# Kernel tuning notes

Hardware: AMD Instinct MI355X
Metric: run time of the kernel (lower is better)

Reference implementation:

```python
import math
import jax, jax.numpy as jnp
import numpy as np

B, S, D, H, DK = 2, 2048, 1024, 16, 64
NUM_BUCKETS, MAX_DISTANCE = 32, 128


def _relative_position_bucket(rel_pos):
    # bidirectional=True (encoder): is_decoder=False
    nb = NUM_BUCKETS // 2
    rel_buckets = (rel_pos > 0).astype(jnp.int32) * nb
    rp = jnp.abs(rel_pos)
    max_exact = nb // 2
    is_small = rp < max_exact
    rp_large = max_exact + (
        jnp.log(rp.astype(jnp.float32) / max_exact)
        / math.log(MAX_DISTANCE / max_exact)
        * (nb - max_exact)
    ).astype(jnp.int32)
    rp_large = jnp.minimum(rp_large, nb - 1)
    return rel_buckets + jnp.where(is_small, rp, rp_large)


def compute_bias(rel_bias, q_len, k_len):
    ctx = jnp.arange(q_len, dtype=jnp.int32)[:, None]
    mem = jnp.arange(k_len, dtype=jnp.int32)[None, :]
    buckets = _relative_position_bucket(mem - ctx)          # [q,k]
    vals = rel_bias[buckets]                                 # [q,k,H]
    return jnp.transpose(vals, (2, 0, 1))[None]              # [1,H,q,k]


def setup_inputs() -> dict:
    key = jax.random.key(0)
    ks = jax.random.split(key, 6)
    scale = 0.02
    return {
        "hidden_states": jax.random.normal(ks[0], (B, S, D), jnp.float32),
        "Wq": jax.random.normal(ks[1], (D, H * DK), jnp.float32) * scale,
        "Wk": jax.random.normal(ks[2], (D, H * DK), jnp.float32) * scale,
        "Wv": jax.random.normal(ks[3], (D, H * DK), jnp.float32) * scale,
        "Wo": jax.random.normal(ks[4], (H * DK, D), jnp.float32) * scale,
        "rel_bias": jax.random.normal(ks[5], (NUM_BUCKETS, H), jnp.float32) * scale,
    }


def reference(hidden_states, Wq, Wk, Wv, Wo, rel_bias):
    b, s, _ = hidden_states.shape

    def shape(x):  # [b,s,H*DK] -> [b,H,s,DK]
        return x.reshape(b, s, H, DK).transpose(0, 2, 1, 3)

    q = shape(hidden_states @ Wq)
    k = shape(hidden_states @ Wk)
    v = shape(hidden_states @ Wv)

    # T5: no 1/sqrt(d_k) scaling
    scores = jnp.einsum("bhqd,bhkd->bhqk", q, k)
    position_bias = compute_bias(rel_bias, s, s)             # [1,H,s,s]
    scores = scores + position_bias
    attn = jax.nn.softmax(scores.astype(jnp.float32), axis=-1).astype(scores.dtype)
    out = jnp.einsum("bhqk,bhkd->bhqd", attn, v)
    out = out.transpose(0, 2, 1, 3).reshape(b, s, H * DK)
    return out @ Wo
```

## Files before the change

kernel.cpp:

```cpp
#include <hip/hip_runtime.h>

#define HH 16
#define DKK 64
#define SS 2048
#define BB 2
#define DD 1024

typedef __attribute__((ext_vector_type(4))) float f32x4;
typedef __attribute__((ext_vector_type(8))) short bf16x8;
typedef __attribute__((ext_vector_type(4))) short s16x4;
typedef __attribute__((ext_vector_type(2))) int i32x2;

#define WAITCNT_VM0 0xF70

__device__ __forceinline__ short bf16b(float f) {
    union { float f; unsigned u; } x; x.f = f;
    unsigned r = (x.u + 0x7fffu + ((x.u >> 16) & 1u)) >> 16;
    return (short)r;
}

__device__ __forceinline__ unsigned f2u(float f) {
    union { float f; unsigned u; } x; x.f = f;
    return x.u;
}

__device__ __forceinline__ f32x4 mfma16(bf16x8 a, bf16x8 b, f32x4 c) {
    return __builtin_amdgcn_mfma_f32_16x16x32_bf16(a, b, c, 0, 0, 0);
}

__device__ __forceinline__ void lds16(const short* g, short* l) {
    __builtin_amdgcn_global_load_lds(
        (const __attribute__((address_space(1))) void*)g,
        (__attribute__((address_space(3))) void*)l, 16, 0, 0);
}

__global__ __launch_bounds__(256) void prep(
    const float* __restrict__ hs,
    const float* __restrict__ W0, const float* __restrict__ W1,
    const float* __restrict__ W2, const float* __restrict__ W3,
    const float* __restrict__ rb,
    short* __restrict__ hsb,
    short* __restrict__ T0, short* __restrict__ T1,
    short* __restrict__ T2, short* __restrict__ T3,
    float* __restrict__ tab) {
    __shared__ short tile[32][33];
    int blk = blockIdx.x, tid = threadIdx.x;
    if (blk < 4096) {
        int i = (blk * 256 + tid) * 4;
        f32x4 v = *(const f32x4*)(hs + i);
        s16x4 o;
        o.x = bf16b(v.x); o.y = bf16b(v.y); o.z = bf16b(v.z); o.w = bf16b(v.w);
        *(s16x4*)(hsb + i) = o;
    } else if (blk < 8192) {
        int t = blk - 4096;
        int z = t >> 10, r = t & 1023;
        int bx = r & 31, by = r >> 5;
        const float* W; short* T;
        switch (z) {
            case 0: W = W0; T = T0; break;
            case 1: W = W1; T = T1; break;
            case 2: W = W2; T = T2; break;
            default: W = W3; T = T3; break;
        }
        int n0 = bx * 32, k0 = by * 32;
        int tx = tid & 31, ty = (tid >> 5) * 4;
#pragma unroll
        for (int i = 0; i < 4; i++)
            tile[ty + i][tx] = bf16b(W[(k0 + ty + i) * DD + n0 + tx]);
        __syncthreads();
#pragma unroll
        for (int i = 0; i < 4; i++)
            T[(n0 + ty + i) * DD + k0 + tx] = tile[tx][ty + i];
    } else {
        int idx = (blk - 8192) * 256 + tid;
        if (idx < HH * 4095) {
            int h = idx / 4095, d = idx % 4095;
            int rel = d - 2047;
            int bucket = (rel > 0) ? 16 : 0;
            unsigned rr = (rel < 0) ? (unsigned)(-rel) : (unsigned)rel;
            int add;
            if (rr < 8) add = (int)rr;
            else {
                int e = 31 - __clz(rr);
                unsigned long long r2 = (unsigned long long)rr * (unsigned long long)rr;
                int f = 2 * e + ((r2 >= (2ull << (2 * e))) ? 1 : 0);
                add = 8 + (f - 6);
                if (add > 15) add = 15;
            }
            bucket += add;
            tab[h * 4095 + d] = rb[bucket * HH + h] * 1.44269504f;
        }
    }
}

__global__ __launch_bounds__(256) void gemm_qkv(
    const short* __restrict__ A, const short* __restrict__ Wt,
    short* __restrict__ Cq, short* __restrict__ Ck, short* __restrict__ Cvt) {
    const int K = 1024;
    __shared__ short As[128 * 32];
    __shared__ short Bs[128 * 32];
    int tid = threadIdx.x;
    int wave = tid >> 6, lane = tid & 63;
    int quad = lane >> 4, l16 = lane & 15;
    int m0 = blockIdx.y * 128, n0 = blockIdx.x * 128;

    int wm = (wave & 1) * 64, wn = (wave >> 1) * 64;
    int r0 = tid >> 2, c0 = (tid & 3) * 8;

    f32x4 acc[4][4];
#pragma unroll
    for (int i = 0; i < 4; i++)
#pragma unroll
        for (int j = 0; j < 4; j++) acc[i][j] = (f32x4){0.f, 0.f, 0.f, 0.f};

    for (int k0 = 0; k0 < K; k0 += 32) {
        __syncthreads();
        lds16(A + (size_t)(m0 + r0) * K + k0 + c0, As + wave * 512);
        lds16(A + (size_t)(m0 + 64 + r0) * K + k0 + c0, As + 2048 + wave * 512);
        lds16(Wt + (size_t)(n0 + r0) * K + k0 + c0, Bs + wave * 512);
        lds16(Wt + (size_t)(n0 + 64 + r0) * K + k0 + c0, Bs + 2048 + wave * 512);
        __syncthreads();
        bf16x8 af[4], bfr[4];
#pragma unroll
        for (int t = 0; t < 4; t++) {
            af[t] = *(const bf16x8*)(As + (wm + t * 16 + l16) * 32 + quad * 8);
            bfr[t] = *(const bf16x8*)(Bs + (wn + t * 16 + l16) * 32 + quad * 8);
        }
#pragma unroll
        for (int mt = 0; mt < 4; mt++)
#pragma unroll
            for (int nt = 0; nt < 4; nt++)
                acc[mt][nt] = mfma16(af[mt], bfr[nt], acc[mt][nt]);
    }

#pragma unroll
    for (int mt = 0; mt < 4; mt++) {
#pragma unroll
        for (int nt = 0; nt < 4; nt++) {
#pragma unroll
            for (int r = 0; r < 4; r++) {
                int gm = m0 + wm + mt * 16 + quad * 4 + r;
                int gn = n0 + wn + nt * 16 + l16;
                int b = gm >> 11, s = gm & 2047;
                int which = gn >> 10;
                int h = (gn >> 6) & 15, dk = gn & 63;
                short bv = bf16b(acc[mt][nt][r]);
                if (which == 0)
                    Cq[(((size_t)(b * HH + h)) * SS + s) * DKK + dk] = bv;
                else if (which == 1)
                    Ck[(((size_t)(b * HH + h)) * SS + s) * DKK + dk] = bv;
                else
                    Cvt[(((size_t)(b * HH + h)) * DKK + dk) * SS + s] = bv;
            }
        }
    }
}

__global__ __launch_bounds__(256) void gemm_out(
    const short* __restrict__ A, const short* __restrict__ Wt,
    float* __restrict__ Cout) {
    const int K = 1024, N = 1024;
    __shared__ short As[64 * 32];
    __shared__ short Bs[128 * 32];
    int tid = threadIdx.x;
    int wave = tid >> 6, lane = tid & 63;
    int quad = lane >> 4, l16 = lane & 15;
    int m0 = blockIdx.y * 64, n0 = blockIdx.x * 128;

    int wm = (wave & 1) * 32, wn = (wave >> 1) * 64;
    int r0 = tid >> 2, c0 = (tid & 3) * 8;

    f32x4 acc[2][4];
#pragma unroll
    for (int i = 0; i < 2; i++)
#pragma unroll
        for (int j = 0; j < 4; j++) acc[i][j] = (f32x4){0.f, 0.f, 0.f, 0.f};

    for (int k0 = 0; k0 < K; k0 += 32) {
        __syncthreads();
        lds16(A + (size_t)(m0 + r0) * K + k0 + c0, As + wave * 512);
        lds16(Wt + (size_t)(n0 + r0) * K + k0 + c0, Bs + wave * 512);
        lds16(Wt + (size_t)(n0 + 64 + r0) * K + k0 + c0, Bs + 2048 + wave * 512);
        __syncthreads();
        bf16x8 af[2], bfr[4];
#pragma unroll
        for (int t = 0; t < 2; t++)
            af[t] = *(const bf16x8*)(As + (wm + t * 16 + l16) * 32 + quad * 8);
#pragma unroll
        for (int t = 0; t < 4; t++)
            bfr[t] = *(const bf16x8*)(Bs + (wn + t * 16 + l16) * 32 + quad * 8);
#pragma unroll
        for (int mt = 0; mt < 2; mt++)
#pragma unroll
            for (int nt = 0; nt < 4; nt++)
                acc[mt][nt] = mfma16(af[mt], bfr[nt], acc[mt][nt]);
    }

#pragma unroll
    for (int mt = 0; mt < 2; mt++)
#pragma unroll
        for (int nt = 0; nt < 4; nt++)
#pragma unroll
            for (int r = 0; r < 4; r++) {
                int gm = m0 + wm + mt * 16 + quad * 4 + r;
                int gn = n0 + wn + nt * 16 + l16;
                Cout[(size_t)gm * N + gn] = acc[mt][nt][r];
            }
}

__global__ __launch_bounds__(256, 4) void attn(
    const short* __restrict__ Q, const short* __restrict__ Kmat,
    const short* __restrict__ Vt, const float* __restrict__ btab,
    short* __restrict__ O) {
    __shared__ short Ks[2][64 * 64];
    __shared__ short Vs[2][64 * 64];
    __shared__ short P_s[4][16 * 64];

    int tid = threadIdx.x;
    int wave = tid >> 6, lane = tid & 63;
    int quad = lane >> 4, l16 = lane & 15;
    int bh = blockIdx.x;
    int h = bh & 15, b = bh >> 4;
    int q0b = blockIdx.y * 64;
    int q0w = q0b + wave * 16;

    const short* Qb = Q + (size_t)bh * SS * DKK;
    const short* Kb = Kmat + (size_t)bh * SS * DKK;
    const short* Vb = Vt + (size_t)bh * DKK * SS;
    const float* bt = btab + h * 4095;

    float blo = bt[2047 - 128];
    float bhi = bt[2047 + 128];

    int kro = tid >> 3;
    int gk = (tid & 7) ^ (kro & 7);
    const short* Kg0 = Kb + (size_t)kro * DKK + gk * 8;
    const short* Kg1 = Kb + (size_t)(kro + 32) * DKK + gk * 8;
    const short* Vg0 = Vb + (size_t)kro * SS + gk * 8;
    const short* Vg1 = Vb + (size_t)(kro + 32) * SS + gk * 8;

    bf16x8 qf0 = *(const bf16x8*)(Qb + (q0w + l16) * DKK + quad * 8);
    bf16x8 qf1 = *(const bf16x8*)(Qb + (q0w + l16) * DKK + 32 + quad * 8);

    f32x4 o[4];
#pragma unroll
    for (int i = 0; i < 4; i++) o[i] = (f32x4){0.f, 0.f, 0.f, 0.f};
    f32x4 lacc = (f32x4){0.f, 0.f, 0.f, 0.f};

    bf16x8 onesf;
    short onev = (l16 == 0) ? (short)0x3F80 : (short)0;
#pragma unroll
    for (int i = 0; i < 8; i++) onesf[i] = onev;

    short* Pw = &P_s[wave][0];
    int gxor = l16 & 7;
    int ghalf = quad >> 1;
    int wbase = l16 * 64 + (quad & 1) * 4;
    int ra0 = l16 * 64 + ((quad ^ gxor) * 8);
    int ra1 = l16 * 64 + (((4 + quad) ^ gxor) * 8);
    int sl0 = (quad ^ gxor) * 8;
    int sl1 = ((4 + quad) ^ gxor) * 8;
    int bq = 2047 + quad * 4 - l16 - q0w;

    lds16(Kg0, &Ks[0][wave * 512]);
    lds16(Kg1, &Ks[0][2048 + wave * 512]);
    lds16(Vg0, &Vs[0][wave * 512]);
    lds16(Vg1, &Vs[0][2048 + wave * 512]);

    int cur = 0;
    for (int kc = 0; kc < SS; kc += 64) {
        __syncthreads();
        int kn = (kc + 64) & (SS - 1);
        int nxt = cur ^ 1;
        lds16(Kg0 + (size_t)kn * DKK, &Ks[nxt][wave * 512]);
        lds16(Kg1 + (size_t)kn * DKK, &Ks[nxt][2048 + wave * 512]);
        lds16(Vg0 + kn, &Vs[nxt][wave * 512]);
        lds16(Vg1 + kn, &Vs[nxt][2048 + wave * 512]);

        float breg[16];
        if (kc > q0w - 191 && kc < q0w + 143) {
#pragma unroll
            for (int kt = 0; kt < 4; kt++)
#pragma unroll
                for (int r = 0; r < 4; r++)
                    breg[kt * 4 + r] = bt[bq + kc + kt * 16 + r];
        } else {
            float bc = (kc <= q0w - 191) ? blo : bhi;
#pragma unroll
            for (int i = 0; i < 16; i++) breg[i] = bc;
        }

        const short* Ksc = &Ks[cur][0];
        const short* Vsc = &Vs[cur][0];

        f32x4 s[4];
#pragma unroll
        for (int kt = 0; kt < 4; kt++) {
            int row = (kt * 16 + l16) * 64;
            bf16x8 kf0 = *(const bf16x8*)(Ksc + row + sl0);
            bf16x8 kf1 = *(const bf16x8*)(Ksc + row + sl1);
            s[kt] = mfma16(kf0, qf0, (f32x4){0.f, 0.f, 0.f, 0.f});
            s[kt] = mfma16(kf1, qf1, s[kt]);
        }
        bf16x8 vf[4][2];
#pragma unroll
        for (int nt = 0; nt < 4; nt++) {
            int row = (nt * 16 + l16) * 64;
            vf[nt][0] = *(const bf16x8*)(Vsc + row + sl0);
            vf[nt][1] = *(const bf16x8*)(Vsc + row + sl1);
        }

#pragma unroll
        for (int kt = 0; kt < 4; kt++) {
            unsigned u[4];
#pragma unroll
            for (int r = 0; r < 4; r++) {
                float p = __builtin_amdgcn_exp2f(
                    fmaf(s[kt][r], 1.44269504f, breg[kt * 4 + r]));
                u[r] = f2u(p) + 0x8000u;
            }
            unsigned d0 = __builtin_amdgcn_perm(u[1], u[0], 0x07060302u);
            unsigned d1 = __builtin_amdgcn_perm(u[3], u[2], 0x07060302u);
            int g = (kt * 2 + ghalf) ^ gxor;
            *(i32x2*)(Pw + wbase + g * 8) = (i32x2){(int)d0, (int)d1};
        }
        __asm__ __volatile__("" ::: "memory");
        {
            bf16x8 pf0 = *(const bf16x8*)(Pw + ra0);
            bf16x8 pf1 = *(const bf16x8*)(Pw + ra1);
            lacc = mfma16(pf0, onesf, lacc);
            lacc = mfma16(pf1, onesf, lacc);
#pragma unroll
            for (int nt = 0; nt < 4; nt++) {
                o[nt] = mfma16(pf0, vf[nt][0], o[nt]);
                o[nt] = mfma16(pf1, vf[nt][1], o[nt]);
            }
        }
        __asm__ __volatile__("" ::: "memory");
        cur ^= 1;
    }
    __builtin_amdgcn_s_waitcnt(WAITCNT_VM0);

    float inv[4];
#pragma unroll
    for (int r = 0; r < 4; r++) {
        float l = __shfl(lacc[r], lane & 48);
        inv[r] = 1.f / l;
    }
#pragma unroll
    for (int nt = 0; nt < 4; nt++)
#pragma unroll
        for (int r = 0; r < 4; r++) {
            int qrow = q0w + quad * 4 + r;
            int dk = nt * 16 + l16;
            O[((size_t)(b * SS + qrow)) * (HH * DKK) + h * DKK + dk] =
                bf16b(o[nt][r] * inv[r]);
        }
}

extern "C" void kernel_launch(void* const* d_in, const int* in_sizes, int n_in,
                              void* d_out, int out_size, void* d_ws, size_t ws_size,
                              hipStream_t stream) {
    const float* hs = (const float*)d_in[0];
    const float* Wq = (const float*)d_in[1];
    const float* Wk = (const float*)d_in[2];
    const float* Wv = (const float*)d_in[3];
    const float* Wo = (const float*)d_in[4];
    const float* rb = (const float*)d_in[5];
    float* out = (float*)d_out;

    char* ws = (char*)d_ws;
    size_t off = 0;
    auto alloc = [&](size_t bytes) -> void* {
        void* p = (void*)(ws + off);
        off += (bytes + 255) & ~(size_t)255;
        return p;
    };
    const size_t M = (size_t)BB * SS;
    short* hsb = (short*)alloc(M * DD * 2);
    short* WqT = (short*)alloc((size_t)DD * DD * 2);
    short* WkT = (short*)alloc((size_t)DD * DD * 2);
    short* WvT = (short*)alloc((size_t)DD * DD * 2);
    short* WoT = (short*)alloc((size_t)DD * DD * 2);
    short* Qb  = (short*)alloc(M * DD * 2);
    short* Kb  = (short*)alloc(M * DD * 2);
    short* VTb = (short*)alloc(M * DD * 2);
    short* Ab  = (short*)alloc(M * DD * 2);
    float* btab = (float*)alloc((size_t)HH * 4095 * 4);

    prep<<<8448, 256, 0, stream>>>(hs, Wq, Wk, Wv, Wo, rb,
                                   hsb, WqT, WkT, WvT, WoT, btab);
    gemm_qkv<<<dim3(24, 32), 256, 0, stream>>>(hsb, WqT, Qb, Kb, VTb);
    attn<<<dim3(32, 32), 256, 0, stream>>>(Qb, Kb, VTb, btab, Ab);
    gemm_out<<<dim3(8, 64), 256, 0, stream>>>(Ab, WoT, out);
}
```

Before: 196.5 us.

## Rewrite attention with 32x32 MFMA tiles and register-resident P via permlane swap

The attention kernel moves from 16x16x32 to 32x32x16 bf16 MFMA, so each wave handles 32 query rows and each block 128. The softmax probabilities are packed with v_cvt_pk_bf16_f32 and rearranged with v_permlane32_swap instead of a round trip through LDS, and the row sums are accumulated with scalar adds instead of an extra MFMA against a ones vector. This is meant to cut LDS traffic and MFMA issue overhead and to raise K/V reuse per block. In exchange it halves the grid, lowers the occupancy target to 2 blocks per CU, and raises register pressure.

```diff
diff --git a/kernel.cpp b/kernel.cpp
--- a/kernel.cpp
+++ b/kernel.cpp
@@ -7,9 +7,10 @@
 #define DD 1024
 
 typedef __attribute__((ext_vector_type(4))) float f32x4;
+typedef __attribute__((ext_vector_type(16))) float f32x16;
 typedef __attribute__((ext_vector_type(8))) short bf16x8;
 typedef __attribute__((ext_vector_type(4))) short s16x4;
-typedef __attribute__((ext_vector_type(2))) int i32x2;
+typedef __attribute__((ext_vector_type(4))) int i32x4;
 
 #define WAITCNT_VM0 0xF70
 
@@ -19,19 +20,28 @@
     return (short)r;
 }
 
-__device__ __forceinline__ unsigned f2u(float f) {
-    union { float f; unsigned u; } x; x.f = f;
-    return x.u;
-}
-
 __device__ __forceinline__ f32x4 mfma16(bf16x8 a, bf16x8 b, f32x4 c) {
     return __builtin_amdgcn_mfma_f32_16x16x32_bf16(a, b, c, 0, 0, 0);
+}
+
+__device__ __forceinline__ f32x16 mfma32(bf16x8 a, bf16x8 b, f32x16 c) {
+    return __builtin_amdgcn_mfma_f32_32x32x16_bf16(a, b, c, 0, 0, 0);
 }
 
 __device__ __forceinline__ void lds16(const short* g, short* l) {
     __builtin_amdgcn_global_load_lds(
         (const __attribute__((address_space(1))) void*)g,
         (__attribute__((address_space(3))) void*)l, 16, 0, 0);
+}
+
+__device__ __forceinline__ int cvtpk(float lo, float hi) {
+    int r;
+    asm("v_cvt_pk_bf16_f32 %0, %1, %2" : "=v"(r) : "v"(lo), "v"(hi));
+    return r;
+}
+
+__device__ __forceinline__ void swap32(int& a, int& b) {
+    asm("v_permlane32_swap_b32 %0, %1" : "+v"(a), "+v"(b));
 }
 
 __global__ __launch_bounds__(256) void prep(
@@ -208,21 +218,22 @@
             }
 }
 
-__global__ __launch_bounds__(256, 4) void attn(
+__global__ __launch_bounds__(256, 2) void attn(
     const short* __restrict__ Q, const short* __restrict__ Kmat,
     const short* __restrict__ Vt, const float* __restrict__ btab,
     short* __restrict__ O) {
     __shared__ short Ks[2][64 * 64];
     __shared__ short Vs[2][64 * 64];
-    __shared__ short P_s[4][16 * 64];
+    __shared__ float Linv[4][32];
 
     int tid = threadIdx.x;
     int wave = tid >> 6, lane = tid & 63;
-    int quad = lane >> 4, l16 = lane & 15;
+    int el = lane & 31, hi = lane >> 5;
+    int ex7 = el & 7;
     int bh = blockIdx.x;
     int h = bh & 15, b = bh >> 4;
-    int q0b = blockIdx.y * 64;
-    int q0w = q0b + wave * 16;
+    int q0b = blockIdx.y * 128;
+    int q0w = q0b + wave * 32;
 
     const short* Qb = Q + (size_t)bh * SS * DKK;
     const short* Kb = Kmat + (size_t)bh * SS * DKK;
@@ -239,28 +250,17 @@
     const short* Vg0 = Vb + (size_t)kro * SS + gk * 8;
     const short* Vg1 = Vb + (size_t)(kro + 32) * SS + gk * 8;
 
-    bf16x8 qf0 = *(const bf16x8*)(Qb + (q0w + l16) * DKK + quad * 8);
-    bf16x8 qf1 = *(const bf16x8*)(Qb + (q0w + l16) * DKK + 32 + quad * 8);
-
-    f32x4 o[4];
-#pragma unroll
-    for (int i = 0; i < 4; i++) o[i] = (f32x4){0.f, 0.f, 0.f, 0.f};
-    f32x4 lacc = (f32x4){0.f, 0.f, 0.f, 0.f};
-
-    bf16x8 onesf;
-    short onev = (l16 == 0) ? (short)0x3F80 : (short)0;
-#pragma unroll
-    for (int i = 0; i < 8; i++) onesf[i] = onev;
-
-    short* Pw = &P_s[wave][0];
-    int gxor = l16 & 7;
-    int ghalf = quad >> 1;
-    int wbase = l16 * 64 + (quad & 1) * 4;
-    int ra0 = l16 * 64 + ((quad ^ gxor) * 8);
-    int ra1 = l16 * 64 + (((4 + quad) ^ gxor) * 8);
-    int sl0 = (quad ^ gxor) * 8;
-    int sl1 = ((4 + quad) ^ gxor) * 8;
-    int bq = 2047 + quad * 4 - l16 - q0w;
+    bf16x8 qB[4];
+#pragma unroll
+    for (int c = 0; c < 4; c++)
+        qB[c] = *(const bf16x8*)(Qb + (size_t)(q0w + el) * DKK + c * 16 + hi * 8);
+
+    f32x16 o0, o1;
+#pragma unroll
+    for (int i = 0; i < 16; i++) { o0[i] = 0.f; o1[i] = 0.f; }
+    float ls0 = 0.f, ls1 = 0.f, ls2 = 0.f, ls3 = 0.f;
+
+    int bq = 2047 - q0w - el;
 
     lds16(Kg0, &Ks[0][wave * 512]);
     lds16(Kg1, &Ks[0][2048 + wave * 512]);
@@ -277,85 +277,83 @@
         lds16(Vg0 + kn, &Vs[nxt][wave * 512]);
         lds16(Vg1 + kn, &Vs[nxt][2048 + wave * 512]);
 
-        float breg[16];
-        if (kc > q0w - 191 && kc < q0w + 143) {
-#pragma unroll
-            for (int kt = 0; kt < 4; kt++)
-#pragma unroll
-                for (int r = 0; r < 4; r++)
-                    breg[kt * 4 + r] = bt[bq + kc + kt * 16 + r];
-        } else {
-            float bc = (kc <= q0w - 191) ? blo : bhi;
-#pragma unroll
-            for (int i = 0; i < 16; i++) breg[i] = bc;
-        }
-
         const short* Ksc = &Ks[cur][0];
         const short* Vsc = &Vs[cur][0];
 
-        f32x4 s[4];
-#pragma unroll
-        for (int kt = 0; kt < 4; kt++) {
-            int row = (kt * 16 + l16) * 64;
-            bf16x8 kf0 = *(const bf16x8*)(Ksc + row + sl0);
-            bf16x8 kf1 = *(const bf16x8*)(Ksc + row + sl1);
-            s[kt] = mfma16(kf0, qf0, (f32x4){0.f, 0.f, 0.f, 0.f});
-            s[kt] = mfma16(kf1, qf1, s[kt]);
-        }
         bf16x8 vf[4][2];
 #pragma unroll
-        for (int nt = 0; nt < 4; nt++) {
-            int row = (nt * 16 + l16) * 64;
-            vf[nt][0] = *(const bf16x8*)(Vsc + row + sl0);
-            vf[nt][1] = *(const bf16x8*)(Vsc + row + sl1);
-        }
-
-#pragma unroll
-        for (int kt = 0; kt < 4; kt++) {
-            unsigned u[4];
-#pragma unroll
-            for (int r = 0; r < 4; r++) {
-                float p = __builtin_amdgcn_exp2f(
-                    fmaf(s[kt][r], 1.44269504f, breg[kt * 4 + r]));
-                u[r] = f2u(p) + 0x8000u;
-            }
-            unsigned d0 = __builtin_amdgcn_perm(u[1], u[0], 0x07060302u);
-            unsigned d1 = __builtin_amdgcn_perm(u[3], u[2], 0x07060302u);
-            int g = (kt * 2 + ghalf) ^ gxor;
-            *(i32x2*)(Pw + wbase + g * 8) = (i32x2){(int)d0, (int)d1};
-        }
-        __asm__ __volatile__("" ::: "memory");
-        {
-            bf16x8 pf0 = *(const bf16x8*)(Pw + ra0);
-            bf16x8 pf1 = *(const bf16x8*)(Pw + ra1);
-            lacc = mfma16(pf0, onesf, lacc);
-            lacc = mfma16(pf1, onesf, lacc);
-#pragma unroll
-            for (int nt = 0; nt < 4; nt++) {
-                o[nt] = mfma16(pf0, vf[nt][0], o[nt]);
-                o[nt] = mfma16(pf1, vf[nt][1], o[nt]);
-            }
-        }
-        __asm__ __volatile__("" ::: "memory");
+        for (int c4 = 0; c4 < 4; c4++)
+#pragma unroll
+            for (int m = 0; m < 2; m++)
+                vf[c4][m] = *(const bf16x8*)(
+                    Vsc + (m * 32 + el) * 64 + (((2 * c4 + hi) ^ ex7) * 8));
+
+#pragma unroll
+        for (int st = 0; st < 2; st++) {
+            f32x16 acc;
+#pragma unroll
+            for (int i = 0; i < 16; i++) acc[i] = 0.f;
+#pragma unroll
+            for (int c = 0; c < 4; c++) {
+                bf16x8 kA = *(const bf16x8*)(
+                    Ksc + (st * 32 + el) * 64 + (((2 * c + hi) ^ ex7) * 8));
+                acc = mfma32(kA, qB[c], acc);
+            }
+
+            int ks = kc + st * 32;
+            float br[16];
+            if (ks > q0w - 159 && ks < q0w + 159) {
+#pragma unroll
+                for (int r = 0; r < 16; r++)
+                    br[r] = bt[bq + ks + ((r & 3) + 8 * (r >> 2) + 4 * hi)];
+            } else {
+                float bc = (ks <= q0w - 159) ? blo : bhi;
+#pragma unroll
+                for (int r = 0; r < 16; r++) br[r] = bc;
+            }
+
+            float p[16];
+#pragma unroll
+            for (int r = 0; r < 16; r++)
+                p[r] = __builtin_amdgcn_exp2f(
+                    fmaf(acc[r], 1.44269504f, br[r]));
+#pragma unroll
+            for (int r = 0; r < 16; r += 4) {
+                ls0 += p[r]; ls1 += p[r + 1]; ls2 += p[r + 2]; ls3 += p[r + 3];
+            }
+
+            int A1 = cvtpk(p[0], p[1]),   A2 = cvtpk(p[2], p[3]);
+            int B1 = cvtpk(p[4], p[5]),   B2 = cvtpk(p[6], p[7]);
+            int C1 = cvtpk(p[8], p[9]),   C2 = cvtpk(p[10], p[11]);
+            int D1 = cvtpk(p[12], p[13]), D2 = cvtpk(p[14], p[15]);
+            swap32(A1, B1); swap32(A2, B2);
+            swap32(C1, D1); swap32(C2, D2);
+            bf16x8 pf0 = __builtin_bit_cast(bf16x8, (i32x4){A1, A2, B1, B2});
+            bf16x8 pf1 = __builtin_bit_cast(bf16x8, (i32x4){C1, C2, D1, D2});
+
+            o0 = mfma32(pf0, vf[st * 2 + 0][0], o0);
+            o1 = mfma32(pf0, vf[st * 2 + 0][1], o1);
+            o0 = mfma32(pf1, vf[st * 2 + 1][0], o0);
+            o1 = mfma32(pf1, vf[st * 2 + 1][1], o1);
+        }
         cur ^= 1;
     }
     __builtin_amdgcn_s_waitcnt(WAITCNT_VM0);
 
-    float inv[4];
-#pragma unroll
-    for (int r = 0; r < 4; r++) {
-        float l = __shfl(lacc[r], lane & 48);
-        inv[r] = 1.f / l;
-    }
-#pragma unroll
-    for (int nt = 0; nt < 4; nt++)
-#pragma unroll
-        for (int r = 0; r < 4; r++) {
-            int qrow = q0w + quad * 4 + r;
-            int dk = nt * 16 + l16;
-            O[((size_t)(b * SS + qrow)) * (HH * DKK) + h * DKK + dk] =
-                bf16b(o[nt][r] * inv[r]);
-        }
+    float lsum = (ls0 + ls1) + (ls2 + ls3);
+    float tot = lsum + __shfl_xor(lsum, 32);
+    float inv = 1.f / tot;
+    if (hi == 0) Linv[wave][el] = inv;
+    __asm__ __volatile__("" ::: "memory");
+
+#pragma unroll
+    for (int r = 0; r < 16; r++) {
+        int qm = (r & 3) + 8 * (r >> 2) + 4 * hi;
+        float iv = Linv[wave][qm];
+        size_t base = ((size_t)(b * SS + q0w + qm)) * (HH * DKK) + h * DKK;
+        O[base + el] = bf16b(o0[r] * iv);
+        O[base + 32 + el] = bf16b(o1[r] * iv);
+    }
 }
 
 extern "C" void kernel_launch(void* const* d_in, const int* in_sizes, int n_in,
@@ -391,6 +389,6 @@
     prep<<<8448, 256, 0, stream>>>(hs, Wq, Wk, Wv, Wo, rb,
                                    hsb, WqT, WkT, WvT, WoT, btab);
     gemm_qkv<<<dim3(24, 32), 256, 0, stream>>>(hsb, WqT, Qb, Kb, VTb);
-    attn<<<dim3(32, 32), 256, 0, stream>>>(Qb, Kb, VTb, btab, Ab);
+    attn<<<dim3(32, 16), 256, 0, stream>>>(Qb, Kb, VTb, btab, Ab);
     gemm_out<<<dim3(8, 64), 256, 0, stream>>>(Ab, WoT, out);
 }
```

New measurement: 193.2 us. Within noise of the previous version (-1.7%).
